# Optimization experiments

Hardware: AMD Instinct MI355X
Metric: run time of the kernel (lower is better)

Reference implementation:

```python
import jax, jax.numpy as jnp
import numpy as np

K = 3          # kernel_size
P = 1          # padding
S = 1          # stride
C_IN = 64
C_OUT = 64


def unfold_patches(t, k=K, p=P, s=S):
    """Replicate-pad then extract kxk patches.
    Input  t: [B, C, H, W]
    Output  : [B, Ho, Wo, C, k*k]  matching torch unfold(2).unfold(3).permute(0,2,3,1,4,5).reshape
    (patch index varies as kh*k + kw)."""
    B, C, H, W = t.shape
    tp = jnp.pad(t, ((0, 0), (0, 0), (p, p), (p, p)), mode='edge')
    Ho = (H + 2 * p - k) // s + 1
    Wo = (W + 2 * p - k) // s + 1
    pats = [tp[:, :, a:a + (Ho - 1) * s + 1:s, b:b + (Wo - 1) * s + 1:s]
            for a in range(k) for b in range(k)]
    y = jnp.stack(pats, axis=-1)          # [B, C, Ho, Wo, k*k]
    return jnp.transpose(y, (0, 2, 3, 1, 4))  # [B, Ho, Wo, C, k*k]


def setup_inputs() -> dict:
    key = jax.random.key(0)
    k1, k2, k3, k4, k5, k6, k7 = jax.random.split(key, 7)
    B, H, W = 4, 128, 128
    feat_in = K * K * C_IN * 2      # 1152
    f1_out = K * K * C_IN           # 576
    f2_out = C_IN * C_OUT           # 4096
    lim1 = 1.0 / np.sqrt(feat_in)
    x = jax.random.normal(k1, (B, C_IN, H, W), dtype=jnp.float32)
    m = jax.random.uniform(k2, (B, C_IN, H, W), dtype=jnp.float32)
    s = jax.random.uniform(k3, (B, C_IN, H, W), dtype=jnp.float32)
    W1 = jax.random.uniform(k4, (feat_in, f1_out), minval=-lim1, maxval=lim1, dtype=jnp.float32)
    b1 = jax.random.uniform(k5, (f1_out,), minval=-lim1, maxval=lim1, dtype=jnp.float32)
    W2 = jax.random.uniform(k6, (feat_in, f2_out), minval=-lim1, maxval=lim1, dtype=jnp.float32)
    b2 = jax.random.uniform(k7, (f2_out,), minval=-lim1, maxval=lim1, dtype=jnp.float32)
    return {"x": x, "m": m, "s": s, "W1": W1, "b1": b1, "W2": W2, "b2": b2}


def reference(x, m, s, W1, b1, W2, b2):
    yp = unfold_patches(x)                              # [B,Ho,Wo,Cin,K2]
    mp = jax.lax.stop_gradient(unfold_patches(m))       # torch no_grad
    sp = jax.lax.stop_gradient(unfold_patches(s))
    B, Ho, Wo = yp.shape[:3]

    feat = jnp.concatenate([yp.reshape(B, Ho, Wo, -1),
                            mp.reshape(B, Ho, Wo, -1)], axis=-1)  # [B,Ho,Wo,2*K2*Cin]
    w1 = (feat @ W1 + b1).reshape(B, Ho, Wo, C_IN, K * K)
    w2 = (feat @ W2 + b2).reshape(B, Ho, Wo, C_IN, C_OUT)

    # y = sum_c (sum_k yp*w1) * w2
    yr = jnp.einsum('bhwck,bhwck->bhwc', yp, w1)
    y = jnp.einsum('bhwc,bhwco->bhwo', yr, w2)
    y = jnp.transpose(y, (0, 3, 1, 2))                  # [B,Cout,Ho,Wo]

    aw1 = jnp.abs(w1)
    aw2 = jnp.abs(w2)
    mr = jnp.einsum('bhwck,bhwck->bhwc', mp, aw1)
    m_y = jnp.transpose(jnp.einsum('bhwc,bhwco->bhwo', mr, aw2), (0, 3, 1, 2))
    sr = jnp.einsum('bhwck,bhwck->bhwc', sp, aw1)
    s_y = jnp.transpose(jnp.einsum('bhwc,bhwco->bhwo', sr, aw2), (0, 3, 1, 2))
    m_y = jax.lax.stop_gradient(m_y / s_y)

    return (y, m_y, jnp.ones_like(m_y))
```

## Files before the change

### kernel.cpp

```cpp
#include <hip/hip_runtime.h>
#include <stdint.h>
#include <stddef.h>


using short8   = __attribute__((ext_vector_type(8))) short;
using float4v  = __attribute__((ext_vector_type(4))) float;
using ushort4v = __attribute__((ext_vector_type(4))) unsigned short;

#define DI __device__ __forceinline__

DI unsigned short f2bf(float f) {
  union { float f; unsigned int u; } a; a.f = f;
  unsigned int r = a.u + 0x7fffu + ((a.u >> 16) & 1u);
  return (unsigned short)(r >> 16);
}
DI float bf2f(unsigned short u) {
  union { unsigned int u; float f; } a; a.u = ((unsigned int)u) << 16;
  return a.f;
}
DI void gll16(const void* g, void* l) {
  __builtin_amdgcn_global_load_lds(
      (const __attribute__((address_space(1))) unsigned int*)g,
      (__attribute__((address_space(3))) unsigned int*)l, 16, 0, 0);
}

__global__ void k_feat(const float* __restrict__ x, const float* __restrict__ m,
                       unsigned short* __restrict__ featb) {
  unsigned int tid = blockIdx.x * 256u + threadIdx.x;
  int j8   = tid & 7;
  int pl   = (tid >> 3) & 127;
  int q    = (tid >> 10) & 3;
  int pblk = (tid >> 12) & 511;
  int kk   = tid >> 21;
  int col  = kk * 32 + q * 8 + j8;
  const float* src = x;
  int jx = col;
  if (col >= 576) { src = m; jx = col - 576; }
  int c  = jx / 9;
  int t  = jx - c * 9;
  int t3 = t / 3;
  int dh = t3 - 1;
  int dw = (t - t3 * 3) - 1;
  int p  = pblk * 128 + pl;
  int b  = p >> 14, h = (p >> 7) & 127, w = p & 127;
  int hh = min(max(h + dh, 0), 127);
  int ww = min(max(w + dw, 0), 127);
  featb[tid] = f2bf(src[(((b << 6) | c) << 14) + (hh << 7) + ww]);
}

__global__ void k_sw(const float* __restrict__ Wsrc, unsigned short* __restrict__ Wdst,
                     int ncols, int ntiles, int total, int perm) {
  int tid = blockIdx.x * 256 + threadIdx.x;
  if (tid >= total) return;
  int k = tid / ncols;
  int n = tid - k * ncols;
  int np = perm ? (((n & 63) << 6) | (n >> 6)) : n;
  int out = ((k >> 5) * ntiles + (np >> 4)) * 512 + ((k >> 3) & 3) * 128 +
            (np & 15) * 8 + (k & 7);
  Wdst[out] = f2bf(Wsrc[tid]);
}

__launch_bounds__(512, 2)
__global__ void k_gemm1(const unsigned short* __restrict__ featb,
                        const unsigned short* __restrict__ W1s,
                        const float* __restrict__ b1,
                        const float* __restrict__ x, const float* __restrict__ m,
                        const float* __restrict__ s,
                        float* __restrict__ yr, float* __restrict__ mr,
                        float* __restrict__ sr) {
  __shared__ __align__(16) unsigned short Alds[4096];
  __shared__ __align__(16) unsigned short Blds[4608];
  __shared__ __align__(16) unsigned short w1buf[128 * 152];
  const int tid = threadIdx.x;
  const int wv  = tid >> 6;
  const int l15 = tid & 15;
  const int q   = (tid >> 4) & 3;
  const int bm  = blockIdx.x, nb = blockIdx.y;

  float4v acc[9];
#pragma unroll
  for (int t = 0; t < 9; ++t) acc[t] = (float4v){0.f, 0.f, 0.f, 0.f};

  const unsigned short* Ab = featb + (size_t)bm * 4096;
  const unsigned short* Bb = W1s + (size_t)nb * 9 * 512;

  for (int kk = 0; kk < 36; ++kk) {
    __syncthreads();
    gll16(Ab + (size_t)kk * 2097152 + tid * 8, (char*)Alds + wv * 1024);
    gll16(Bb + (size_t)kk * 18432 + tid * 8, (char*)Blds + wv * 1024);
    if (tid < 64) gll16(Bb + (size_t)kk * 18432 + 4096 + tid * 8, (char*)Blds + 8192);
    __syncthreads();
    short8 af = *(const short8*)&Alds[q * 1024 + (16 * wv + l15) * 8];
#pragma unroll
    for (int t = 0; t < 9; ++t) {
      short8 bfr = *(const short8*)&Blds[t * 512 + q * 128 + l15 * 8];
      acc[t] = __builtin_amdgcn_mfma_f32_16x16x32_bf16(af, bfr, acc[t], 0, 0, 0);
    }
  }

#pragma unroll
  for (int t = 0; t < 9; ++t) {
    int col = 16 * t + l15;
    float bb = b1[nb * 144 + col];
#pragma unroll
    for (int i = 0; i < 4; ++i) {
      int plr = 16 * wv + 4 * q + i;
      w1buf[plr * 152 + col] = f2bf(acc[t][i] + bb);
    }
  }
  __syncthreads();

  const int b = bm >> 7, h = bm & 127;
#pragma unroll
  for (int ii = 0; ii < 4; ++ii) {
    int task = ii * 512 + tid;
    int p  = task >> 4;
    int cl = task & 15;
    int c  = nb * 16 + cl;
    float w1v[9];
#pragma unroll
    for (int k = 0; k < 9; ++k) w1v[k] = bf2f(w1buf[p * 152 + cl * 9 + k]);
    size_t base = (size_t)(((b << 6) | c) << 14);
    float vy = 0.f, vm = 0.f, vs = 0.f;
#pragma unroll
    for (int dh = -1; dh <= 1; ++dh) {
      int hh = min(max(h + dh, 0), 127);
#pragma unroll
      for (int dw = -1; dw <= 1; ++dw) {
        int ww = min(max(p + dw, 0), 127);
        size_t idx = base + (hh << 7) + ww;
        int k = (dh + 1) * 3 + (dw + 1);
        float wv1 = w1v[k], aw = fabsf(wv1);
        vy += x[idx] * wv1;
        vm += m[idx] * aw;
        vs += s[idx] * aw;
      }
    }
    size_t P = (size_t)bm * 128 + p;
    yr[P * 64 + c] = vy;
    mr[P * 64 + c] = vm;
    sr[P * 64 + c] = vs;
  }
}

__launch_bounds__(512, 4)
__global__ void k_gemm2(const unsigned short* __restrict__ featb,
                        const unsigned short* __restrict__ W2s,
                        const float* __restrict__ b2,
                        const float* __restrict__ yr, const float* __restrict__ mr,
                        const float* __restrict__ sr,
                        float* __restrict__ out) {
  __shared__ __align__(16) unsigned short U[3][12288];
  unsigned short* w2buf = &U[2][0];
  const int tid  = threadIdx.x;
  const int wv   = tid >> 6;
  const int lane = tid & 63;
  const int wm   = wv >> 2;
  const int wn   = wv & 3;
  const int l15  = tid & 15;
  const int q    = (tid >> 4) & 3;
  const int part = lane >> 4;
  const int bm   = blockIdx.x;

  const unsigned short* Ab = featb + (size_t)bm * 4096;

  float4v acc[4][4];
#pragma unroll
  for (int r = 0; r < 4; ++r)
#pragma unroll
    for (int t = 0; t < 4; ++t) acc[r][t] = (float4v){0.f, 0.f, 0.f, 0.f};

  gll16(Ab + tid * 8,                  (char*)&U[0][0]    + wv * 1024);
  gll16(W2s + tid * 8,                 (char*)&U[0][4096] + wv * 1024);
  gll16(W2s + 4096 + tid * 8,          (char*)&U[0][8192] + wv * 1024);
  gll16(Ab + 2097152 + tid * 8,        (char*)&U[1][0]    + wv * 1024);
  gll16(W2s + 131072 + tid * 8,        (char*)&U[1][4096] + wv * 1024);
  gll16(W2s + 131072 + 4096 + tid * 8, (char*)&U[1][8192] + wv * 1024);

#define G2_KK(KK, BR, BS, DRAIN)                                               \
  do {                                                                         \
    int kks = (KK) + 2, chs = ch;                                              \
    if (kks >= 36) { kks -= 36; chs += 1; }                                    \
    if (DRAIN) { asm volatile("s_waitcnt vmcnt(0)" ::: "memory"); }            \
    else       { asm volatile("s_waitcnt vmcnt(3)" ::: "memory"); }            \
    __builtin_amdgcn_s_barrier();                                              \
    asm volatile("" ::: "memory");                                             \
    if (chs < 16) {                                                            \
      const unsigned short* Ag = Ab + (size_t)kks * 2097152;                   \
      const unsigned short* Bg = W2s + (size_t)kks * 131072 + (size_t)chs * 8192; \
      gll16(Ag + tid * 8,        (char*)&U[BS][0]    + wv * 1024);             \
      gll16(Bg + tid * 8,        (char*)&U[BS][4096] + wv * 1024);             \
      gll16(Bg + 4096 + tid * 8, (char*)&U[BS][8192] + wv * 1024);             \
    }                                                                          \
    {                                                                          \
      const unsigned short* Al = &U[BR][0];                                    \
      const unsigned short* Bl = &U[BR][4096];                                 \
      short8 a_[4];                                                            \
      _Pragma("unroll") for (int r = 0; r < 4; ++r)                            \
        a_[r] = *(const short8*)&Al[q * 1024 + (64 * wm + 16 * r + l15) * 8];  \
      __builtin_amdgcn_s_setprio(1);                                           \
      _Pragma("unroll") for (int t = 0; t < 4; ++t) {                          \
        short8 bfr = *(const short8*)&Bl[(4 * wn + t) * 512 + q * 128 + l15 * 8]; \
        _Pragma("unroll") for (int r = 0; r < 4; ++r)                          \
          acc[r][t] = __builtin_amdgcn_mfma_f32_16x16x32_bf16(a_[r], bfr,      \
                                                              acc[r][t], 0, 0, 0); \
      }                                                                        \
      __builtin_amdgcn_s_setprio(0);                                           \
    }                                                                          \
  } while (0)

  for (int ch = 0; ch < 16; ++ch) {
    const bool lc = (ch == 15);
    for (int k3 = 0; k3 < 12; ++k3) {
      const int kk = k3 * 3;
      G2_KK(kk + 0, 0, 2, false);
      G2_KK(kk + 1, 1, 0, (lc && k3 == 11));
      G2_KK(kk + 2, 2, 1, (lc && k3 == 11));
    }

    float b2v[4];
#pragma unroll
    for (int t = 0; t < 4; ++t) b2v[t] = b2[(16 * t + l15) * 64 + 4 * ch + wn];

    for (int p = 0; p < 4; ++p) {
      __syncthreads();
      if (wn == p) {
#pragma unroll
        for (int r = 0; r < 4; ++r)
#pragma unroll
          for (int t = 0; t < 4; ++t)
#pragma unroll
            for (int i = 0; i < 4; ++i)
              w2buf[(64 * wm + 16 * r + 4 * q + i) * 68 + 16 * t + l15] =
                  f2bf(acc[r][t][i] + b2v[t]);
      }
      __syncthreads();
      const int row = 16 * wv + l15;
      const size_t P = (size_t)bm * 128 + row;
      const float4v* y4 = (const float4v*)(yr + P * 64 + 16 * part);
      const float4v* m4 = (const float4v*)(mr + P * 64 + 16 * part);
      const float4v* s4 = (const float4v*)(sr + P * 64 + 16 * part);
      const ushort4v* w4 = (const ushort4v*)&w2buf[row * 68 + 16 * part];
      float ys = 0.f, ms = 0.f, ss = 0.f;
#pragma unroll
      for (int j4 = 0; j4 < 4; ++j4) {
        float4v yv = y4[j4], mv = m4[j4], sv = s4[j4];
        ushort4v wq = w4[j4];
#pragma unroll
        for (int j = 0; j < 4; ++j) {
          float w2f = bf2f(wq[j]);
          float aw  = fabsf(w2f);
          ys += yv[j] * w2f;
          ms += mv[j] * aw;
          ss += sv[j] * aw;
        }
      }
      ys += __shfl_xor(ys, 16); ys += __shfl_xor(ys, 32);
      ms += __shfl_xor(ms, 16); ms += __shfl_xor(ms, 32);
      ss += __shfl_xor(ss, 16); ss += __shfl_xor(ss, 32);
      if (part == 0) {
        const int o = 4 * ch + p;
        const int b = (int)(P >> 14), h = (int)((P >> 7) & 127), w = (int)(P & 127);
        size_t idx = ((size_t)((b << 6) | o) << 14) + (h << 7) + w;
        out[idx]           = ys;
        out[4194304 + idx] = ms / ss;
        out[8388608 + idx] = 1.0f;
      }
    }
#pragma unroll
    for (int r = 0; r < 4; ++r)
#pragma unroll
      for (int t = 0; t < 4; ++t) acc[r][t] = (float4v){0.f, 0.f, 0.f, 0.f};
  }
#undef G2_KK
}

extern "C" void kernel_launch(void* const* d_in, const int* in_sizes, int n_in,
                              void* d_out, int out_size, void* d_ws, size_t ws_size,
                              hipStream_t stream) {
  const float* x  = (const float*)d_in[0];
  const float* m  = (const float*)d_in[1];
  const float* s  = (const float*)d_in[2];
  const float* W1 = (const float*)d_in[3];
  const float* b1 = (const float*)d_in[4];
  const float* W2 = (const float*)d_in[5];
  const float* b2 = (const float*)d_in[6];
  float* out = (float*)d_out;

  if (ws_size < 212090880ull) return;
  char* ws = (char*)d_ws;
  unsigned short* featb = (unsigned short*)ws;
  unsigned short* W1s   = (unsigned short*)(ws + 150994944);
  unsigned short* W2s   = (unsigned short*)(ws + 152322048);
  float* yr = (float*)(ws + 161759232);
  float* mr = (float*)(ws + 178536448);
  float* sr = (float*)(ws + 195313664);

  k_feat<<<294912, 256, 0, stream>>>(x, m, featb);
  k_sw<<<2592, 256, 0, stream>>>(W1, W1s, 576, 36, 663552, 0);
  k_sw<<<18432, 256, 0, stream>>>(W2, W2s, 4096, 256, 4718592, 1);
  dim3 g1(512, 4);
  k_gemm1<<<g1, 512, 0, stream>>>(featb, W1s, b1, x, m, s, yr, mr, sr);
  k_gemm2<<<512, 512, 0, stream>>>(featb, W2s, b2, yr, mr, sr, out);
}
```

Measured before the change: 1.242 ms.

## Triple-buffer gemm1 LDS pipeline and stream gemm2 B operand via registers

gemm1 moves from a single-buffered load/sync/compute loop to a three-stage LDS ring with async global-to-LDS prefetch two steps ahead, and shrinks LDS so four blocks per CU fit. gemm2 stops staging W2 tiles in LDS. Each wave loads its B fragments straight from global memory into double-buffered registers one step ahead, and only the A tile stays in the LDS ring. This aims to hide memory latency and cut LDS traffic and footprint, at the cost of more register pressure and uncoalesced, redundant global reads of W2 across the block's waves.

```diff
diff --git a/kernel.cpp b/kernel.cpp
--- a/kernel.cpp
+++ b/kernel.cpp
@@ -60,7 +60,7 @@
   Wdst[out] = f2bf(Wsrc[tid]);
 }
 
-__launch_bounds__(512, 2)
+__launch_bounds__(512, 4)
 __global__ void k_gemm1(const unsigned short* __restrict__ featb,
                         const unsigned short* __restrict__ W1s,
                         const float* __restrict__ b1,
@@ -68,9 +68,8 @@
                         const float* __restrict__ s,
                         float* __restrict__ yr, float* __restrict__ mr,
                         float* __restrict__ sr) {
-  __shared__ __align__(16) unsigned short Alds[4096];
-  __shared__ __align__(16) unsigned short Blds[4608];
-  __shared__ __align__(16) unsigned short w1buf[128 * 152];
+  __shared__ __align__(16) unsigned short U[3][8704];
+  unsigned short* w1buf = &U[0][0];
   const int tid = threadIdx.x;
   const int wv  = tid >> 6;
   const int l15 = tid & 15;
@@ -84,19 +83,53 @@
   const unsigned short* Ab = featb + (size_t)bm * 4096;
   const unsigned short* Bb = W1s + (size_t)nb * 9 * 512;
 
-  for (int kk = 0; kk < 36; ++kk) {
-    __syncthreads();
-    gll16(Ab + (size_t)kk * 2097152 + tid * 8, (char*)Alds + wv * 1024);
-    gll16(Bb + (size_t)kk * 18432 + tid * 8, (char*)Blds + wv * 1024);
-    if (tid < 64) gll16(Bb + (size_t)kk * 18432 + 4096 + tid * 8, (char*)Blds + 8192);
-    __syncthreads();
-    short8 af = *(const short8*)&Alds[q * 1024 + (16 * wv + l15) * 8];
-#pragma unroll
-    for (int t = 0; t < 9; ++t) {
-      short8 bfr = *(const short8*)&Blds[t * 512 + q * 128 + l15 * 8];
-      acc[t] = __builtin_amdgcn_mfma_f32_16x16x32_bf16(af, bfr, acc[t], 0, 0, 0);
-    }
-  }
+  gll16(Ab + tid * 8, (char*)&U[0][0] + wv * 1024);
+  gll16(Bb + tid * 8, (char*)&U[0][4096] + wv * 1024);
+  if (tid < 64) gll16(Bb + 4096 + tid * 8, (char*)&U[0][8192]);
+  gll16(Ab + 2097152 + tid * 8, (char*)&U[1][0] + wv * 1024);
+  gll16(Bb + 18432 + tid * 8, (char*)&U[1][4096] + wv * 1024);
+  if (tid < 64) gll16(Bb + 18432 + 4096 + tid * 8, (char*)&U[1][8192]);
+
+#define G1_STEP(KK, BR, BS, HEADW)                                             \
+  do {                                                                         \
+    asm volatile("s_waitcnt vmcnt(" #HEADW ")" ::: "memory");                  \
+    __builtin_amdgcn_s_barrier();                                              \
+    asm volatile("" ::: "memory");                                             \
+    {                                                                          \
+      int kks = (KK) + 2;                                                      \
+      if (kks < 36) {                                                          \
+        gll16(Ab + (size_t)kks * 2097152 + tid * 8, (char*)&U[BS][0] + wv * 1024); \
+        gll16(Bb + (size_t)kks * 18432 + tid * 8, (char*)&U[BS][4096] + wv * 1024); \
+        if (tid < 64)                                                          \
+          gll16(Bb + (size_t)kks * 18432 + 4096 + tid * 8, (char*)&U[BS][8192]); \
+      }                                                                        \
+    }                                                                          \
+    {                                                                          \
+      short8 af = *(const short8*)&U[BR][q * 1024 + (16 * wv + l15) * 8];      \
+      __builtin_amdgcn_s_setprio(1);                                           \
+      _Pragma("unroll") for (int t = 0; t < 9; ++t) {                          \
+        short8 bfr = *(const short8*)&U[BR][4096 + t * 512 + q * 128 + l15 * 8]; \
+        acc[t] = __builtin_amdgcn_mfma_f32_16x16x32_bf16(af, bfr, acc[t], 0, 0, 0); \
+      }                                                                        \
+      __builtin_amdgcn_s_setprio(0);                                           \
+    }                                                                          \
+  } while (0)
+
+  G1_STEP(0, 0, 2, 2);
+  G1_STEP(1, 1, 0, 2);
+  G1_STEP(2, 2, 1, 2);
+  for (int k3 = 1; k3 < 11; ++k3) {
+    const int kk = 3 * k3;
+    G1_STEP(kk + 0, 0, 2, 2);
+    G1_STEP(kk + 1, 1, 0, 2);
+    G1_STEP(kk + 2, 2, 1, 2);
+  }
+  G1_STEP(33, 0, 2, 2);
+  G1_STEP(34, 1, 0, 2);
+  G1_STEP(35, 2, 1, 0);
+#undef G1_STEP
+
+  __syncthreads();
 
 #pragma unroll
   for (int t = 0; t < 9; ++t) {
@@ -150,8 +183,8 @@
                         const float* __restrict__ yr, const float* __restrict__ mr,
                         const float* __restrict__ sr,
                         float* __restrict__ out) {
-  __shared__ __align__(16) unsigned short U[3][12288];
-  unsigned short* w2buf = &U[2][0];
+  __shared__ __align__(16) unsigned short U[3][4096];
+  __shared__ __align__(16) unsigned short w2buf[128 * 68];
   const int tid  = threadIdx.x;
   const int wv   = tid >> 6;
   const int lane = tid & 63;
@@ -163,6 +196,7 @@
   const int bm   = blockIdx.x;
 
   const unsigned short* Ab = featb + (size_t)bm * 4096;
+  const int boff = wn * 2048 + q * 128 + l15 * 8;
 
   float4v acc[4][4];
 #pragma unroll
@@ -170,52 +204,74 @@
 #pragma unroll
     for (int t = 0; t < 4; ++t) acc[r][t] = (float4v){0.f, 0.f, 0.f, 0.f};
 
-  gll16(Ab + tid * 8,                  (char*)&U[0][0]    + wv * 1024);
-  gll16(W2s + tid * 8,                 (char*)&U[0][4096] + wv * 1024);
-  gll16(W2s + 4096 + tid * 8,          (char*)&U[0][8192] + wv * 1024);
-  gll16(Ab + 2097152 + tid * 8,        (char*)&U[1][0]    + wv * 1024);
-  gll16(W2s + 131072 + tid * 8,        (char*)&U[1][4096] + wv * 1024);
-  gll16(W2s + 131072 + 4096 + tid * 8, (char*)&U[1][8192] + wv * 1024);
-
-#define G2_KK(KK, BR, BS, DRAIN)                                               \
+  short8 b0_[4], b1_[4];
+
+  gll16(Ab + tid * 8, (char*)&U[0][0] + wv * 1024);
+  gll16(Ab + 2097152 + tid * 8, (char*)&U[1][0] + wv * 1024);
+  asm volatile("" ::: "memory");
+  {
+    const unsigned short* Bg = W2s + boff;
+#pragma unroll
+    for (int t = 0; t < 4; ++t) b0_[t] = *(const short8*)(Bg + t * 512);
+  }
+
+#define G2_STEP(KK, BR, BS, BC, BN, HEADW)                                     \
   do {                                                                         \
-    int kks = (KK) + 2, chs = ch;                                              \
-    if (kks >= 36) { kks -= 36; chs += 1; }                                    \
-    if (DRAIN) { asm volatile("s_waitcnt vmcnt(0)" ::: "memory"); }            \
-    else       { asm volatile("s_waitcnt vmcnt(3)" ::: "memory"); }            \
+    asm volatile("s_waitcnt vmcnt(" #HEADW ")" ::: "memory");                  \
     __builtin_amdgcn_s_barrier();                                              \
     asm volatile("" ::: "memory");                                             \
-    if (chs < 16) {                                                            \
-      const unsigned short* Ag = Ab + (size_t)kks * 2097152;                   \
-      const unsigned short* Bg = W2s + (size_t)kks * 131072 + (size_t)chs * 8192; \
-      gll16(Ag + tid * 8,        (char*)&U[BS][0]    + wv * 1024);             \
-      gll16(Bg + tid * 8,        (char*)&U[BS][4096] + wv * 1024);             \
-      gll16(Bg + 4096 + tid * 8, (char*)&U[BS][8192] + wv * 1024);             \
+    {                                                                          \
+      int kkB = (KK) + 1, chB = ch;                                            \
+      if (kkB >= 36) { kkB -= 36; chB += 1; }                                  \
+      if (chB < 16) {                                                          \
+        const unsigned short* Bg =                                             \
+            W2s + (size_t)kkB * 131072 + (size_t)chB * 8192 + boff;            \
+        _Pragma("unroll") for (int t = 0; t < 4; ++t)                          \
+          BN[t] = *(const short8*)(Bg + t * 512);                              \
+      }                                                                        \
+      int kks = (KK) + 2, chs = ch;                                            \
+      if (kks >= 36) { kks -= 36; chs += 1; }                                  \
+      if (chs < 16)                                                            \
+        gll16(Ab + (size_t)kks * 2097152 + tid * 8, (char*)&U[BS][0] + wv * 1024); \
     }                                                                          \
     {                                                                          \
-      const unsigned short* Al = &U[BR][0];                                    \
-      const unsigned short* Bl = &U[BR][4096];                                 \
       short8 a_[4];                                                            \
       _Pragma("unroll") for (int r = 0; r < 4; ++r)                            \
-        a_[r] = *(const short8*)&Al[q * 1024 + (64 * wm + 16 * r + l15) * 8];  \
+        a_[r] = *(const short8*)&U[BR][q * 1024 + (64 * wm + 16 * r + l15) * 8]; \
       __builtin_amdgcn_s_setprio(1);                                           \
-      _Pragma("unroll") for (int t = 0; t < 4; ++t) {                          \
-        short8 bfr = *(const short8*)&Bl[(4 * wn + t) * 512 + q * 128 + l15 * 8]; \
+      _Pragma("unroll") for (int t = 0; t < 4; ++t)                            \
         _Pragma("unroll") for (int r = 0; r < 4; ++r)                          \
-          acc[r][t] = __builtin_amdgcn_mfma_f32_16x16x32_bf16(a_[r], bfr,      \
+          acc[r][t] = __builtin_amdgcn_mfma_f32_16x16x32_bf16(a_[r], BC[t],    \
                                                               acc[r][t], 0, 0, 0); \
-      }                                                                        \
       __builtin_amdgcn_s_setprio(0);                                           \
     }                                                                          \
   } while (0)
 
   for (int ch = 0; ch < 16; ++ch) {
-    const bool lc = (ch == 15);
-    for (int k3 = 0; k3 < 12; ++k3) {
-      const int kk = k3 * 3;
-      G2_KK(kk + 0, 0, 2, false);
-      G2_KK(kk + 1, 1, 0, (lc && k3 == 11));
-      G2_KK(kk + 2, 2, 1, (lc && k3 == 11));
+    G2_STEP(0, 0, 2, b0_, b1_, 1);
+    G2_STEP(1, 1, 0, b1_, b0_, 5);
+    G2_STEP(2, 2, 1, b0_, b1_, 5);
+    G2_STEP(3, 0, 2, b1_, b0_, 5);
+    G2_STEP(4, 1, 0, b0_, b1_, 5);
+    G2_STEP(5, 2, 1, b1_, b0_, 5);
+    for (int k6 = 1; k6 < 5; ++k6) {
+      const int kk = k6 * 6;
+      G2_STEP(kk + 0, 0, 2, b0_, b1_, 5);
+      G2_STEP(kk + 1, 1, 0, b1_, b0_, 5);
+      G2_STEP(kk + 2, 2, 1, b0_, b1_, 5);
+      G2_STEP(kk + 3, 0, 2, b1_, b0_, 5);
+      G2_STEP(kk + 4, 1, 0, b0_, b1_, 5);
+      G2_STEP(kk + 5, 2, 1, b1_, b0_, 5);
+    }
+    G2_STEP(30, 0, 2, b0_, b1_, 5);
+    G2_STEP(31, 1, 0, b1_, b0_, 5);
+    G2_STEP(32, 2, 1, b0_, b1_, 5);
+    G2_STEP(33, 0, 2, b1_, b0_, 5);
+    G2_STEP(34, 1, 0, b0_, b1_, 5);
+    if (ch < 15) {
+      G2_STEP(35, 2, 1, b1_, b0_, 5);
+    } else {
+      G2_STEP(35, 2, 1, b1_, b0_, 0);
     }
 
     float b2v[4];
@@ -272,7 +328,7 @@
 #pragma unroll
       for (int t = 0; t < 4; ++t) acc[r][t] = (float4v){0.f, 0.f, 0.f, 0.f};
   }
-#undef G2_KK
+#undef G2_STEP
 }
 
 extern "C" void kernel_launch(void* const* d_in, const int* in_sizes, int n_in,
```

Result: slower. 2.622 ms (+111.1%).
